# Optimization experiments

Measured on AMD Instinct MI355X. Metric: run time of the kernel, lower is better.

## Reference

```python
import math
import jax, jax.numpy as jnp
import numpy as np

B, L, D = 8, 4096, 512
FACTOR = 5


def setup_inputs() -> dict:
    key = jax.random.key(0)
    kq, kk, kv = jax.random.split(key, 3)
    q = jax.random.normal(kq, (B, L, D), dtype=jnp.float32)
    k = jax.random.normal(kk, (B, L, D), dtype=jnp.float32)
    v = jax.random.normal(kv, (B, L, D), dtype=jnp.float32)
    return {"q": q, "k": k, "v": v}


def reference(q, k, v):
    # ProbSparse attention (sparse=True branch, L_Q > 1)
    L_Q = q.shape[1]
    scale = q.shape[-1] ** -0.5
    # scores: [B, L_Q, L_K]
    scores = jnp.einsum('bqd,bkd->bqk', q, k) * scale
    # sparsity measure M = max - mean over keys: [B, L_Q]
    M = scores.max(axis=-1) - scores.mean(axis=-1)
    u = max(1, int(FACTOR * math.log(L_Q + 1)))
    u = min(u, L_Q)  # static python int (u = 41 here)
    _, top_idx = jax.lax.top_k(M, u)  # [B, u]
    # gather top-u query rows of scores, softmax over keys (row-wise softmax
    # commutes with row selection, so this matches softmax-then-gather)
    scores_top = jnp.take_along_axis(scores, top_idx[:, :, None], axis=1)  # [B, u, L_K]
    attn = jax.nn.softmax(scores_top, axis=-1)
    out_top = jnp.einsum('buk,bkd->bud', attn, v)  # [B, u, D]
    # non-selected queries receive the mean value
    v_mean = jnp.broadcast_to(v.mean(axis=1, keepdims=True), v.shape)  # [B, L, D]
    b_idx = jnp.arange(q.shape[0])[:, None]  # [B, 1]
    out = v_mean.at[b_idx, top_idx].set(out_top)
    return out
```

## Files before the change

### kernel.cpp

```cpp
#include <hip/hip_runtime.h>
#include <math.h>

#define B_ 8
#define L_ 4096
#define D_ 512
#define U_ 41
#define NSL 16

static constexpr float SCALE = 0.044194173824159216f;

typedef __attribute__((ext_vector_type(8))) short bf16x8;
typedef __attribute__((ext_vector_type(4))) float f32x4;
typedef unsigned int uint;


__global__ __launch_bounds__(512) void kSums1(const float* __restrict__ k,
                                              const float* __restrict__ v,
                                              float* __restrict__ partk,
                                              float* __restrict__ partv) {
  const int s = blockIdx.x;
  const int b = blockIdx.y;
  const int d = threadIdx.x;
  const int rows = L_ / NSL;
  const size_t base = ((size_t)b * L_ + (size_t)s * rows) * D_ + d;
  float ks = 0.f, vs = 0.f;
  for (int l = 0; l < rows; ++l) {
    ks += k[base + (size_t)l * D_];
    vs += v[base + (size_t)l * D_];
  }
  partk[(b * NSL + s) * D_ + d] = ks;
  partv[(b * NSL + s) * D_ + d] = vs;
}

__global__ __launch_bounds__(512) void kSums2(const float* __restrict__ partk,
                                              const float* __restrict__ partv,
                                              float* __restrict__ ksum,
                                              float* __restrict__ vmean) {
  const int b = blockIdx.x;
  const int d = threadIdx.x;
  float ks = 0.f, vs = 0.f;
  for (int s = 0; s < NSL; ++s) {
    ks += partk[(b * NSL + s) * D_ + d];
    vs += partv[(b * NSL + s) * D_ + d];
  }
  ksum[b * D_ + d] = ks;
  vmean[b * D_ + d] = vs * (1.f / L_);
}

__global__ __launch_bounds__(256) void kMeanM(const float* __restrict__ q,
                                              const float* __restrict__ ksum,
                                              const float* __restrict__ pmax,
                                              float* __restrict__ M) {
  __shared__ float ks[D_];
  const int gid = blockIdx.x * 256 + threadIdx.x;
  const int b = gid >> 12;
  for (int i = threadIdx.x; i < D_; i += 256) ks[i] = ksum[b * D_ + i];
  __syncthreads();
  const float* qp = q + (size_t)gid * D_;
  float acc = 0.f;
  for (int i = 0; i < D_; i += 4) {
    float4 t = *(const float4*)(qp + i);
    acc += t.x * ks[i] + t.y * ks[i + 1] + t.z * ks[i + 2] + t.w * ks[i + 3];
  }
  const float rowmax = fmaxf(pmax[gid], pmax[B_ * L_ + gid]);
  M[gid] = SCALE * (rowmax - acc * (1.f / L_));
}

__global__ __launch_bounds__(64) void kTopK2(const float* __restrict__ M,
                                             int* __restrict__ topidx) {
  __shared__ float vals[L_];
  const int b = blockIdx.x;
  const int lane = threadIdx.x;
  for (int i = lane; i < L_; i += 64) vals[i] = M[b * L_ + i];
  __syncthreads();
  for (int it = 0; it < U_; ++it) {
    float bv = -3.4e38f;
    int bi = 0x7fffffff;
    for (int i = lane; i < L_; i += 64) {
      float x = vals[i];
      if (x > bv) { bv = x; bi = i; }
    }
#pragma unroll
    for (int off = 1; off < 64; off <<= 1) {
      float ov = __shfl_xor(bv, off);
      int oi = __shfl_xor(bi, off);
      if (ov > bv || (ov == bv && oi < bi)) { bv = ov; bi = oi; }
    }
    if (lane == 0) { topidx[b * U_ + it] = bi; vals[bi] = -3.4e38f; }
    __syncthreads();
  }
}

__global__ __launch_bounds__(256) void kFill(const float* __restrict__ vmean,
                                             float* __restrict__ out) {
  const int g = blockIdx.x * 256 + threadIdx.x;
  const int d4 = g & 127;
  const int bl = g >> 7;
  const int b = bl >> 12;
  ((float4*)out)[g] = ((const float4*)vmean)[b * 128 + d4];
}

__device__ inline uint bf16_rne_bits(float x) {
  uint u = __builtin_bit_cast(uint, x);
  return (u + 0x7FFFu + ((u >> 16) & 1u)) >> 16;
}
__device__ inline float bits_to_f32(uint hi16) {
  return __builtin_bit_cast(float, hi16 << 16);
}

__global__ __launch_bounds__(256) void kConvert(const float* __restrict__ src,
                                                unsigned char* __restrict__ dhi,
                                                unsigned char* __restrict__ dlo) {
  const int cid = blockIdx.x * 256 + threadIdx.x;
  const int c16 = cid & 7;
  const int row = (cid >> 3) & 127;
  const int dsi = (cid >> 10) & 7;
  const int rt = (cid >> 13) & 31;
  const int b = cid >> 18;
  const int l = rt * 128 + row;
  const int d = dsi * 64 + c16 * 8;
  const float* sp = src + ((size_t)(b * L_ + l) * D_ + d);
  float x[8];
  *(float4*)(x) = *(const float4*)sp;
  *(float4*)(x + 4) = *(const float4*)(sp + 4);
  uint hw[4], lw[4];
#pragma unroll
  for (int p = 0; p < 4; ++p) {
    float a = x[2 * p], c = x[2 * p + 1];
    uint ha = bf16_rne_bits(a), hc = bf16_rne_bits(c);
    float ra = a - bits_to_f32(ha);
    float rc = c - bits_to_f32(hc);
    uint la = bf16_rne_bits(ra), lc = bf16_rne_bits(rc);
    hw[p] = ha | (hc << 16);
    lw[p] = la | (lc << 16);
  }
  const size_t dstByte = ((size_t)(cid >> 3) << 7) +
                         (uint)((c16 << 4) ^ ((row & 7) << 4));
  *(uint4*)(dhi + dstByte) = make_uint4(hw[0], hw[1], hw[2], hw[3]);
  *(uint4*)(dlo + dstByte) = make_uint4(lw[0], lw[1], lw[2], lw[3]);
}

__device__ __forceinline__ void gload16(const unsigned char* g, unsigned char* l) {
  __builtin_amdgcn_global_load_lds(
      (const __attribute__((address_space(1))) unsigned int*)(g),
      (__attribute__((address_space(3))) unsigned int*)(l), 16, 0, 0);
}

__global__ __launch_bounds__(256, 2) void kRowMaxB(const unsigned char* __restrict__ qhi,
                                                   const unsigned char* __restrict__ qlo,
                                                   const unsigned char* __restrict__ khi,
                                                   const unsigned char* __restrict__ klo,
                                                   float* __restrict__ pmax) {
  __shared__ unsigned char lds[65536];
  __shared__ float red[256];
  unsigned char* ldsQhi = lds;
  unsigned char* ldsQlo = lds + 16384;
  unsigned char* ldsKhi = lds + 32768;
  unsigned char* ldsKlo = lds + 49152;

  const int b = blockIdx.y;
  const int qt = blockIdx.x;
  const int kh = blockIdx.z;
  const int tid = threadIdx.x;
  const int lane = tid & 63;
  const int wave = tid >> 6;
  const int wq = wave >> 1, wk = wave & 1;

  const size_t qtb = ((size_t)((b * 32 + qt) * 8)) * 16384;
  const unsigned char* qhB = qhi + qtb;
  const unsigned char* qlB = qlo + qtb;

  float rmax[4][4];
#pragma unroll
  for (int i = 0; i < 4; ++i)
#pragma unroll
    for (int j = 0; j < 4; ++j) rmax[i][j] = -3.4e38f;

  for (int kt = 0; kt < 16; ++kt) {
    const size_t ktb = ((size_t)((b * 32 + (kh * 16 + kt)) * 8)) * 16384;
    const unsigned char* khB = khi + ktb;
    const unsigned char* klB = klo + ktb;

    f32x4 acc[4][4];
#pragma unroll
    for (int i = 0; i < 4; ++i)
#pragma unroll
      for (int j = 0; j < 4; ++j)
#pragma unroll
        for (int e = 0; e < 4; ++e) acc[i][j][e] = 0.f;

    for (int dsi = 0; dsi < 8; ++dsi) {
      __syncthreads();
      {
        const size_t dof = (size_t)dsi * 16384 + (size_t)tid * 16;
        const size_t lof = (size_t)tid * 16;
#pragma unroll
        for (int i = 0; i < 4; ++i) {
          gload16(qhB + dof + i * 4096, ldsQhi + lof + i * 4096);
          gload16(qlB + dof + i * 4096, ldsQlo + lof + i * 4096);
          gload16(khB + dof + i * 4096, ldsKhi + lof + i * 4096);
          gload16(klB + dof + i * 4096, ldsKlo + lof + i * 4096);
        }
      }
      __syncthreads();

#pragma unroll
      for (int h = 0; h < 2; ++h) {
        const int rbyte = h * 64 + ((lane >> 4) << 4);
        bf16x8 aH[4], aL[4], bH[4], bL[4];
#pragma unroll
        for (int f = 0; f < 4; ++f) {
          const int qrow = wq * 64 + f * 16 + (lane & 15);
          const int krow = wk * 64 + f * 16 + (lane & 15);
          const int qoff = qrow * 128 + (rbyte ^ ((qrow & 7) << 4));
          const int koff = krow * 128 + (rbyte ^ ((krow & 7) << 4));
          aH[f] = *(const bf16x8*)(ldsQhi + qoff);
          aL[f] = *(const bf16x8*)(ldsQlo + qoff);
          bH[f] = *(const bf16x8*)(ldsKhi + koff);
          bL[f] = *(const bf16x8*)(ldsKlo + koff);
        }
#pragma unroll
        for (int mf = 0; mf < 4; ++mf)
#pragma unroll
          for (int nf = 0; nf < 4; ++nf) {
            acc[mf][nf] = __builtin_amdgcn_mfma_f32_16x16x32_bf16(aH[mf], bH[nf], acc[mf][nf], 0, 0, 0);
            acc[mf][nf] = __builtin_amdgcn_mfma_f32_16x16x32_bf16(aH[mf], bL[nf], acc[mf][nf], 0, 0, 0);
            acc[mf][nf] = __builtin_amdgcn_mfma_f32_16x16x32_bf16(aL[mf], bH[nf], acc[mf][nf], 0, 0, 0);
          }
      }
    }
#pragma unroll
    for (int mf = 0; mf < 4; ++mf)
#pragma unroll
      for (int r = 0; r < 4; ++r) {
        float m = fmaxf(fmaxf(acc[mf][0][r], acc[mf][1][r]),
                        fmaxf(acc[mf][2][r], acc[mf][3][r]));
        rmax[mf][r] = fmaxf(rmax[mf][r], m);
      }
  }

#pragma unroll
  for (int mf = 0; mf < 4; ++mf)
#pragma unroll
    for (int r = 0; r < 4; ++r) {
      float v = rmax[mf][r];
#pragma unroll
      for (int off = 1; off < 16; off <<= 1) v = fmaxf(v, __shfl_xor(v, off));
      rmax[mf][r] = v;
    }

  if ((lane & 15) == 0) {
#pragma unroll
    for (int mf = 0; mf < 4; ++mf)
#pragma unroll
      for (int r = 0; r < 4; ++r) {
        const int rowl = wq * 64 + mf * 16 + ((lane >> 4) << 2) + r;
        red[wk * 128 + rowl] = rmax[mf][r];
      }
  }
  __syncthreads();
  if (tid < 128) {
    pmax[(size_t)kh * B_ * L_ + (size_t)b * L_ + blockIdx.x * 128 + tid] =
        fmaxf(red[tid], red[128 + tid]);
  }
}


__global__ __launch_bounds__(64) void kGatherQ(const float* __restrict__ q,
                                               const int* __restrict__ topidx,
                                               unsigned char* __restrict__ qselhi,
                                               unsigned char* __restrict__ qsello) {
  const int j = blockIdx.x;
  const int b = blockIdx.y;
  const int lane = threadIdx.x;
  const int dsi = lane >> 3;
  const int c16 = lane & 7;
  float x[8] = {0.f, 0.f, 0.f, 0.f, 0.f, 0.f, 0.f, 0.f};
  if (j < U_) {
    const int row = topidx[b * U_ + j];
    const float* sp = q + ((size_t)(b * L_ + row)) * D_ + dsi * 64 + c16 * 8;
    *(float4*)(x) = *(const float4*)sp;
    *(float4*)(x + 4) = *(const float4*)(sp + 4);
  }
  uint hw[4], lw[4];
#pragma unroll
  for (int p = 0; p < 4; ++p) {
    float a = x[2 * p], c = x[2 * p + 1];
    uint ha = bf16_rne_bits(a), hc = bf16_rne_bits(c);
    float ra = a - bits_to_f32(ha);
    float rc = c - bits_to_f32(hc);
    uint la = bf16_rne_bits(ra), lc = bf16_rne_bits(rc);
    hw[p] = ha | (hc << 16);
    lw[p] = la | (lc << 16);
  }
  const size_t dstByte = ((size_t)((b * 8 + dsi) * 64 + j)) * 128 +
                         (uint)((c16 << 4) ^ ((j & 7) << 4));
  *(uint4*)(qselhi + dstByte) = make_uint4(hw[0], hw[1], hw[2], hw[3]);
  *(uint4*)(qsello + dstByte) = make_uint4(lw[0], lw[1], lw[2], lw[3]);
}

__global__ __launch_bounds__(256) void kSelScoresM(const unsigned char* __restrict__ qselhi,
                                                   const unsigned char* __restrict__ qsello,
                                                   const unsigned char* __restrict__ khi,
                                                   const unsigned char* __restrict__ klo,
                                                   float* __restrict__ P) {
  __shared__ unsigned char lds[49152];
  unsigned char* ldsQhi = lds;
  unsigned char* ldsQlo = lds + 8192;
  unsigned char* ldsKhi = lds + 16384;
  unsigned char* ldsKlo = lds + 32768;

  const int kc = blockIdx.x;
  const int b = blockIdx.y;
  const int tid = threadIdx.x;
  const int lane = tid & 63;
  const int wave = tid >> 6;
  const int wq = wave >> 1, wk = wave & 1;

  const size_t ktb = ((size_t)((b * 32 + kc) * 8)) * 16384;
  const unsigned char* khB = khi + ktb;
  const unsigned char* klB = klo + ktb;
  const size_t qb = ((size_t)b * 8) * 8192;
  const unsigned char* qhB = qselhi + qb;
  const unsigned char* qlB = qsello + qb;

  f32x4 acc[2][4];
#pragma unroll
  for (int i = 0; i < 2; ++i)
#pragma unroll
    for (int j = 0; j < 4; ++j)
#pragma unroll
      for (int e = 0; e < 4; ++e) acc[i][j][e] = 0.f;

  for (int dsi = 0; dsi < 8; ++dsi) {
    __syncthreads();
    {
      const size_t qof = (size_t)dsi * 8192 + (size_t)tid * 16;
      const size_t kof = (size_t)dsi * 16384 + (size_t)tid * 16;
      const size_t lof = (size_t)tid * 16;
#pragma unroll
      for (int i = 0; i < 2; ++i) {
        gload16(qhB + qof + i * 4096, ldsQhi + lof + i * 4096);
        gload16(qlB + qof + i * 4096, ldsQlo + lof + i * 4096);
      }
#pragma unroll
      for (int i = 0; i < 4; ++i) {
        gload16(khB + kof + i * 4096, ldsKhi + lof + i * 4096);
        gload16(klB + kof + i * 4096, ldsKlo + lof + i * 4096);
      }
    }
    __syncthreads();

#pragma unroll
    for (int h = 0; h < 2; ++h) {
      const int rbyte = h * 64 + ((lane >> 4) << 4);
      bf16x8 aH[2], aL[2], bH[4], bL[4];
#pragma unroll
      for (int f = 0; f < 2; ++f) {
        const int qrow = wq * 32 + f * 16 + (lane & 15);
        const int qoff = qrow * 128 + (rbyte ^ ((qrow & 7) << 4));
        aH[f] = *(const bf16x8*)(ldsQhi + qoff);
        aL[f] = *(const bf16x8*)(ldsQlo + qoff);
      }
#pragma unroll
      for (int f = 0; f < 4; ++f) {
        const int krow = wk * 64 + f * 16 + (lane & 15);
        const int koff = krow * 128 + (rbyte ^ ((krow & 7) << 4));
        bH[f] = *(const bf16x8*)(ldsKhi + koff);
        bL[f] = *(const bf16x8*)(ldsKlo + koff);
      }
#pragma unroll
      for (int mf = 0; mf < 2; ++mf)
#pragma unroll
        for (int nf = 0; nf < 4; ++nf) {
          acc[mf][nf] = __builtin_amdgcn_mfma_f32_16x16x32_bf16(aH[mf], bH[nf], acc[mf][nf], 0, 0, 0);
          acc[mf][nf] = __builtin_amdgcn_mfma_f32_16x16x32_bf16(aH[mf], bL[nf], acc[mf][nf], 0, 0, 0);
          acc[mf][nf] = __builtin_amdgcn_mfma_f32_16x16x32_bf16(aL[mf], bH[nf], acc[mf][nf], 0, 0, 0);
        }
    }
  }

#pragma unroll
  for (int mf = 0; mf < 2; ++mf)
#pragma unroll
    for (int nf = 0; nf < 4; ++nf)
#pragma unroll
      for (int r = 0; r < 4; ++r) {
        const int row = wq * 32 + mf * 16 + ((lane >> 4) << 2) + r;
        const int key = kc * 128 + wk * 64 + nf * 16 + (lane & 15);
        if (row < U_)
          P[((size_t)(b * U_ + row)) * L_ + key] = acc[mf][nf][r];
      }
}

__global__ __launch_bounds__(256) void kSoftmaxP(float* __restrict__ P) {
  __shared__ float red[256];
  const int j = blockIdx.x, b = blockIdx.y;
  float* row = P + ((size_t)(b * U_ + j)) * L_;
  const int tid = threadIdx.x;
  float v[16];
  float mx = -3.4e38f;
#pragma unroll
  for (int i = 0; i < 16; ++i) {
    v[i] = row[tid + i * 256];
    mx = fmaxf(mx, v[i]);
  }
  red[tid] = mx;
  __syncthreads();
  for (int s = 128; s > 0; s >>= 1) {
    if (tid < s) red[tid] = fmaxf(red[tid], red[tid + s]);
    __syncthreads();
  }
  mx = red[0];
  __syncthreads();
  float sum = 0.f;
#pragma unroll
  for (int i = 0; i < 16; ++i) {
    float e = expf((v[i] - mx) * SCALE);
    v[i] = e;
    sum += e;
  }
  red[tid] = sum;
  __syncthreads();
  for (int s = 128; s > 0; s >>= 1) {
    if (tid < s) red[tid] += red[tid + s];
    __syncthreads();
  }
  const float inv = 1.f / red[0];
#pragma unroll
  for (int i = 0; i < 16; ++i) row[tid + i * 256] = v[i] * inv;
}

__global__ __launch_bounds__(256) void kPV(const float* __restrict__ P,
                                           const float* __restrict__ v,
                                           float* __restrict__ partial) {
  __shared__ float plds[41 * 128];
  const int kc = blockIdx.x;
  const int dc = blockIdx.y;
  const int b = blockIdx.z;
  const int tid = threadIdx.x;
  const int trow = tid >> 7, dcol = tid & 127;
  float acc[U_];
#pragma unroll
  for (int j = 0; j < U_; ++j) acc[j] = 0.f;

  for (int sub = 0; sub < 4; ++sub) {
    const int key0 = kc * 512 + sub * 128;
    __syncthreads();
    for (int idx = tid; idx < U_ * 128; idx += 256)
      plds[idx] = P[((size_t)(b * U_ + (idx >> 7))) * L_ + key0 + (idx & 127)];
    __syncthreads();
    const float* vp = v + ((size_t)(b * L_ + key0 + trow * 64)) * D_ + dc * 128 + dcol;
    float vv[64];
#pragma unroll
    for (int kk = 0; kk < 64; ++kk) vv[kk] = vp[(size_t)kk * D_];
#pragma unroll
    for (int j = 0; j < U_; ++j) {
      const float4* pr = (const float4*)&plds[j * 128 + trow * 64];
      float a = acc[j];
#pragma unroll
      for (int q4 = 0; q4 < 16; ++q4) {
        float4 p4 = pr[q4];
        a = fmaf(p4.x, vv[q4 * 4 + 0], a);
        a = fmaf(p4.y, vv[q4 * 4 + 1], a);
        a = fmaf(p4.z, vv[q4 * 4 + 2], a);
        a = fmaf(p4.w, vv[q4 * 4 + 3], a);
      }
      acc[j] = a;
    }
  }
  float* pp = partial + ((size_t)((b * 4 + dc) * 16 + kc * 2 + trow)) * (U_ * 128) + dcol;
#pragma unroll
  for (int j = 0; j < U_; ++j) pp[j * 128] = acc[j];
}

__global__ __launch_bounds__(256) void kPVout(const float* __restrict__ partial,
                                              const int* __restrict__ topidx,
                                              float* __restrict__ out) {
  const int j = blockIdx.x, b = blockIdx.y;
  const int tid = threadIdx.x;
  const int l = topidx[b * U_ + j];
#pragma unroll
  for (int h = 0; h < 2; ++h) {
    const int d = tid + h * 256;
    const int dc = d >> 7, dcol = d & 127;
    float s = 0.f;
#pragma unroll
    for (int part = 0; part < 16; ++part)
      s += partial[((size_t)((b * 4 + dc) * 16 + part)) * (U_ * 128) + j * 128 + dcol];
    out[((size_t)(b * L_ + l)) * D_ + d] = s;
  }
}


__device__ inline void stageHalfRow(const float* __restrict__ src,
                                    char* hiBase, char* loBase,
                                    int row, int shalf) {
  const int sw = (row & 7) << 4;
  char* hp = hiBase + row * 128;
  char* lp = loBase + row * 128;
#pragma unroll
  for (int g = 0; g < 4; ++g) {
    f32x4 x0 = *(const f32x4*)(src + g * 8);
    f32x4 x1 = *(const f32x4*)(src + g * 8 + 4);
    float x[8] = {x0.x, x0.y, x0.z, x0.w, x1.x, x1.y, x1.z, x1.w};
    uint hw[4], lw[4];
#pragma unroll
    for (int p = 0; p < 4; ++p) {
      float a = x[2 * p], c = x[2 * p + 1];
      uint ha = bf16_rne_bits(a), hc = bf16_rne_bits(c);
      float ra = a - bits_to_f32(ha);
      float rc = c - bits_to_f32(hc);
      uint la = bf16_rne_bits(ra), lc = bf16_rne_bits(rc);
      hw[p] = ha | (hc << 16);
      lw[p] = la | (lc << 16);
    }
    const int off = (shalf * 64 + g * 16) ^ sw;
    *(uint4*)(hp + off) = make_uint4(hw[0], hw[1], hw[2], hw[3]);
    *(uint4*)(lp + off) = make_uint4(lw[0], lw[1], lw[2], lw[3]);
  }
}

__global__ __launch_bounds__(256, 2) void kRowMaxM(const float* __restrict__ q,
                                                   const float* __restrict__ k,
                                                   float* __restrict__ pmax) {
  __shared__ char lds[65536];
  __shared__ float red[256];
  char* ldsQhi = lds;
  char* ldsQlo = lds + 16384;
  char* ldsKhi = lds + 32768;
  char* ldsKlo = lds + 49152;

  const int b = blockIdx.y;
  const int qbase = blockIdx.x * 128;
  const int kh = blockIdx.z;
  const int tid = threadIdx.x;
  const int lane = tid & 63;
  const int wave = tid >> 6;
  const int wq = wave >> 1, wk = wave & 1;
  const int srow = tid >> 1;
  const int shalf = tid & 1;

  const float* qrow_base = q + ((size_t)b * L_ + qbase + srow) * D_ + shalf * 32;
  const float* krow_base = k + ((size_t)b * L_ + kh * 2048 + srow) * D_ + shalf * 32;

  float rmax[4][4];
#pragma unroll
  for (int i = 0; i < 4; ++i)
#pragma unroll
    for (int j = 0; j < 4; ++j) rmax[i][j] = -3.4e38f;

  for (int kt = 0; kt < 16; ++kt) {
    f32x4 acc[4][4];
#pragma unroll
    for (int i = 0; i < 4; ++i)
#pragma unroll
      for (int j = 0; j < 4; ++j)
#pragma unroll
        for (int e = 0; e < 4; ++e) acc[i][j][e] = 0.f;

    for (int dsi = 0; dsi < 8; ++dsi) {
      __syncthreads();
      stageHalfRow(qrow_base + dsi * 64, ldsQhi, ldsQlo, srow, shalf);
      stageHalfRow(krow_base + (size_t)kt * 128 * D_ + dsi * 64, ldsKhi, ldsKlo, srow, shalf);
      __syncthreads();

#pragma unroll
      for (int h = 0; h < 2; ++h) {
        const int rbyte = h * 64 + ((lane >> 4) << 4);
        bf16x8 aH[4], aL[4], bH[4], bL[4];
#pragma unroll
        for (int f = 0; f < 4; ++f) {
          const int qrow = wq * 64 + f * 16 + (lane & 15);
          const int krow = wk * 64 + f * 16 + (lane & 15);
          const int qoff = qrow * 128 + (rbyte ^ ((qrow & 7) << 4));
          const int koff = krow * 128 + (rbyte ^ ((krow & 7) << 4));
          aH[f] = *(const bf16x8*)(ldsQhi + qoff);
          aL[f] = *(const bf16x8*)(ldsQlo + qoff);
          bH[f] = *(const bf16x8*)(ldsKhi + koff);
          bL[f] = *(const bf16x8*)(ldsKlo + koff);
        }
#pragma unroll
        for (int mf = 0; mf < 4; ++mf)
#pragma unroll
          for (int nf = 0; nf < 4; ++nf) {
            acc[mf][nf] = __builtin_amdgcn_mfma_f32_16x16x32_bf16(aH[mf], bH[nf], acc[mf][nf], 0, 0, 0);
            acc[mf][nf] = __builtin_amdgcn_mfma_f32_16x16x32_bf16(aH[mf], bL[nf], acc[mf][nf], 0, 0, 0);
            acc[mf][nf] = __builtin_amdgcn_mfma_f32_16x16x32_bf16(aL[mf], bH[nf], acc[mf][nf], 0, 0, 0);
          }
      }
    }
#pragma unroll
    for (int mf = 0; mf < 4; ++mf)
#pragma unroll
      for (int r = 0; r < 4; ++r) {
        float m = fmaxf(fmaxf(acc[mf][0][r], acc[mf][1][r]),
                        fmaxf(acc[mf][2][r], acc[mf][3][r]));
        rmax[mf][r] = fmaxf(rmax[mf][r], m);
      }
  }

#pragma unroll
  for (int mf = 0; mf < 4; ++mf)
#pragma unroll
    for (int r = 0; r < 4; ++r) {
      float v = rmax[mf][r];
#pragma unroll
      for (int off = 1; off < 16; off <<= 1) v = fmaxf(v, __shfl_xor(v, off));
      rmax[mf][r] = v;
    }

  if ((lane & 15) == 0) {
#pragma unroll
    for (int mf = 0; mf < 4; ++mf)
#pragma unroll
      for (int r = 0; r < 4; ++r) {
        const int rowl = wq * 64 + mf * 16 + ((lane >> 4) << 2) + r;
        red[wk * 128 + rowl] = rmax[mf][r];
      }
  }
  __syncthreads();
  if (tid < 128) {
    pmax[(size_t)kh * B_ * L_ + (size_t)b * L_ + qbase + tid] =
        fmaxf(red[tid], red[128 + tid]);
  }
}

__global__ __launch_bounds__(256) void kAttnSel(const float* __restrict__ q,
                                                const float* __restrict__ k,
                                                const float* __restrict__ v,
                                                const int* __restrict__ topidx,
                                                float* __restrict__ out) {
  __shared__ float qs[D_];
  __shared__ float sc[L_];
  __shared__ float wred[4];
  __shared__ float sred[256];
  const int b = blockIdx.y;
  const int l_sel = topidx[b * U_ + blockIdx.x];
  const int tid = threadIdx.x;
  const int wave = tid >> 6, lane = tid & 63;
  const float* qrow = q + ((size_t)b * L_ + l_sel) * D_;
  qs[tid] = qrow[tid];
  qs[tid + 256] = qrow[tid + 256];
  __syncthreads();
  float qr[8];
#pragma unroll
  for (int i = 0; i < 8; ++i) qr[i] = qs[lane * 8 + i];
  float wmax = -3.4e38f;
  for (int l = wave; l < L_; l += 4) {
    const float* kp = k + ((size_t)b * L_ + l) * D_ + lane * 8;
    float4 k0 = *(const float4*)kp;
    float4 k1 = *(const float4*)(kp + 4);
    float p = k0.x * qr[0] + k0.y * qr[1] + k0.z * qr[2] + k0.w * qr[3] +
              k1.x * qr[4] + k1.y * qr[5] + k1.z * qr[6] + k1.w * qr[7];
#pragma unroll
    for (int off = 32; off > 0; off >>= 1) p += __shfl_xor(p, off);
    if (lane == 0) sc[l] = p;
    wmax = fmaxf(wmax, p);
  }
  if (lane == 0) wred[wave] = wmax;
  __syncthreads();
  const float mx = fmaxf(fmaxf(wred[0], wred[1]), fmaxf(wred[2], wred[3]));
  float psum = 0.f;
  for (int i = tid; i < L_; i += 256) {
    float e = expf((sc[i] - mx) * SCALE);
    sc[i] = e;
    psum += e;
  }
  sred[tid] = psum;
  __syncthreads();
  for (int s = 128; s > 0; s >>= 1) {
    if (tid < s) sred[tid] += sred[tid + s];
    __syncthreads();
  }
  const float inv = 1.f / sred[0];
  float a0a = 0.f, a0b = 0.f, a1a = 0.f, a1b = 0.f;
  const float* vb = v + (size_t)b * L_ * D_;
  for (int l = 0; l < L_; l += 2) {
    float p0 = sc[l], p1 = sc[l + 1];
    const float* vp0 = vb + (size_t)l * D_;
    const float* vp1 = vp0 + D_;
    a0a = fmaf(p0, vp0[tid], a0a);
    a1a = fmaf(p0, vp0[tid + 256], a1a);
    a0b = fmaf(p1, vp1[tid], a0b);
    a1b = fmaf(p1, vp1[tid + 256], a1b);
  }
  float* orow = out + ((size_t)b * L_ + l_sel) * D_;
  orow[tid] = (a0a + a0b) * inv;
  orow[tid + 256] = (a1a + a1b) * inv;
}


extern "C" void kernel_launch(void* const* d_in, const int* in_sizes, int n_in,
                              void* d_out, int out_size, void* d_ws, size_t ws_size,
                              hipStream_t stream) {
  const float* q = (const float*)d_in[0];
  const float* k = (const float*)d_in[1];
  const float* v = (const float*)d_in[2];
  float* out = (float*)d_out;
  unsigned char* wsb = (unsigned char*)d_ws;

  const size_t NEED = 84183040;

  if (ws_size >= NEED) {
    unsigned char* qhiW = wsb;
    unsigned char* qloW = wsb + 33554432;
    float* pmax = (float*)(wsb + 67108864);
    float* Marr = (float*)(wsb + 67371008);
    float* ksum = (float*)(wsb + 67502080);
    float* vmean = (float*)(wsb + 67518464);
    int* tidx = (int*)(wsb + 67534848);
    float* partk = (float*)(wsb + 67536896);
    float* partv = (float*)(wsb + 67799040);
    float* P = (float*)(wsb + 68061184);
    float* partial = (float*)(wsb + 73435136);
    unsigned char* qselhi = (unsigned char*)partial;
    unsigned char* qsello = qselhi + 524288;
    unsigned char* khiO = (unsigned char*)d_out;
    unsigned char* kloO = khiO + 33554432;

    kConvert<<<8192, 256, 0, stream>>>(q, qhiW, qloW);
    kConvert<<<8192, 256, 0, stream>>>(k, khiO, kloO);
    kSums1<<<dim3(NSL, B_), 512, 0, stream>>>(k, v, partk, partv);
    kSums2<<<B_, 512, 0, stream>>>(partk, partv, ksum, vmean);
    kRowMaxB<<<dim3(L_ / 128, B_, 2), 256, 0, stream>>>(qhiW, qloW, khiO, kloO, pmax);
    kMeanM<<<B_ * L_ / 256, 256, 0, stream>>>(q, ksum, pmax, Marr);
    kTopK2<<<B_, 64, 0, stream>>>(Marr, tidx);
    kGatherQ<<<dim3(64, B_), 64, 0, stream>>>(q, tidx, qselhi, qsello);
    kSelScoresM<<<dim3(32, B_), 256, 0, stream>>>(qselhi, qsello, khiO, kloO, P);
    kSoftmaxP<<<dim3(U_, B_), 256, 0, stream>>>(P);
    kFill<<<B_ * L_ * D_ / 1024, 256, 0, stream>>>(vmean, out);
    kPV<<<dim3(8, 4, B_), 256, 0, stream>>>(P, v, partial);
    kPVout<<<dim3(U_, B_), 256, 0, stream>>>(partial, tidx, out);
  } else {
    float* ws = (float*)d_ws;
    float* Marr = ws;
    float* pmax = ws + 32768;
    float* ksum = ws + 98304;
    float* vmean = ws + 102400;
    int* tidx = (int*)(ws + 106496);
    float* partk = ws + 107008;
    float* partv = ws + 107008 + B_ * NSL * D_;

    kSums1<<<dim3(NSL, B_), 512, 0, stream>>>(k, v, partk, partv);
    kSums2<<<B_, 512, 0, stream>>>(partk, partv, ksum, vmean);
    kRowMaxM<<<dim3(L_ / 128, B_, 2), 256, 0, stream>>>(q, k, pmax);
    kMeanM<<<B_ * L_ / 256, 256, 0, stream>>>(q, ksum, pmax, Marr);
    kTopK2<<<B_, 64, 0, stream>>>(Marr, tidx);
    kFill<<<B_ * L_ * D_ / 1024, 256, 0, stream>>>(vmean, out);
    kAttnSel<<<dim3(U_, B_), 256, 0, stream>>>(q, k, v, tidx, out);
  }
}
```

Baseline: 685.9 us.

## Double-buffer row-max GEMM loads, swizzle workgroups, and register-resident top-k

```diff
diff --git a/kernel.cpp b/kernel.cpp
--- a/kernel.cpp
+++ b/kernel.cpp
@@ -66,28 +66,56 @@
   M[gid] = SCALE * (rowmax - acc * (1.f / L_));
 }
 
-__global__ __launch_bounds__(64) void kTopK2(const float* __restrict__ M,
-                                             int* __restrict__ topidx) {
-  __shared__ float vals[L_];
+__global__ __launch_bounds__(256) void kTopK3(const float* __restrict__ M,
+                                              int* __restrict__ topidx) {
+  __shared__ float wv[2][4];
+  __shared__ int wi[2][4];
   const int b = blockIdx.x;
-  const int lane = threadIdx.x;
-  for (int i = lane; i < L_; i += 64) vals[i] = M[b * L_ + i];
-  __syncthreads();
+  const int tid = threadIdx.x;
+  const int wave = tid >> 6, lane = tid & 63;
+  float v[16];
+#pragma unroll
+  for (int j = 0; j < 16; ++j) v[j] = M[b * L_ + tid + j * 256];
+  float bv = v[0];
+  int bj = 0;
+#pragma unroll
+  for (int j = 1; j < 16; ++j)
+    if (v[j] > bv) { bv = v[j]; bj = j; }
+  int bi = tid + bj * 256;
+
   for (int it = 0; it < U_; ++it) {
-    float bv = -3.4e38f;
-    int bi = 0x7fffffff;
-    for (int i = lane; i < L_; i += 64) {
-      float x = vals[i];
-      if (x > bv) { bv = x; bi = i; }
-    }
+    float rv = bv;
+    int ri = bi;
 #pragma unroll
     for (int off = 1; off < 64; off <<= 1) {
-      float ov = __shfl_xor(bv, off);
-      int oi = __shfl_xor(bi, off);
-      if (ov > bv || (ov == bv && oi < bi)) { bv = ov; bi = oi; }
-    }
-    if (lane == 0) { topidx[b * U_ + it] = bi; vals[bi] = -3.4e38f; }
-    __syncthreads();
+      float ov = __shfl_xor(rv, off);
+      int oi = __shfl_xor(ri, off);
+      if (ov > rv || (ov == rv && oi < ri)) { rv = ov; ri = oi; }
+    }
+    const int par = it & 1;
+    if (lane == 0) { wv[par][wave] = rv; wi[par][wave] = ri; }
+    __syncthreads();
+    float gv = wv[par][0];
+    int gi = wi[par][0];
+#pragma unroll
+    for (int w = 1; w < 4; ++w) {
+      float ov = wv[par][w];
+      int oi = wi[par][w];
+      if (ov > gv || (ov == gv && oi < gi)) { gv = ov; gi = oi; }
+    }
+    if (tid == 0) topidx[b * U_ + it] = gi;
+    if (gi == bi) {
+      const int jb = gi >> 8;
+#pragma unroll
+      for (int j = 0; j < 16; ++j)
+        if (j == jb) v[j] = -3.4e38f;
+      bv = v[0];
+      bj = 0;
+#pragma unroll
+      for (int j = 1; j < 16; ++j)
+        if (v[j] > bv) { bv = v[j]; bj = j; }
+      bi = tid + bj * 256;
+    }
   }
 }
 
@@ -146,97 +174,101 @@
       (__attribute__((address_space(3))) unsigned int*)(l), 16, 0, 0);
 }
 
-__global__ __launch_bounds__(256, 2) void kRowMaxB(const unsigned char* __restrict__ qhi,
+__global__ __launch_bounds__(256, 1) void kRowMaxC(const unsigned char* __restrict__ qhi,
                                                    const unsigned char* __restrict__ qlo,
                                                    const unsigned char* __restrict__ khi,
                                                    const unsigned char* __restrict__ klo,
                                                    float* __restrict__ pmax) {
-  __shared__ unsigned char lds[65536];
-  __shared__ float red[256];
-  unsigned char* ldsQhi = lds;
-  unsigned char* ldsQlo = lds + 16384;
-  unsigned char* ldsKhi = lds + 32768;
-  unsigned char* ldsKlo = lds + 49152;
-
-  const int b = blockIdx.y;
-  const int qt = blockIdx.x;
-  const int kh = blockIdx.z;
+  __shared__ unsigned char lds[131072];
+
+  const int wg = blockIdx.x;
+  const int swz = (wg & 7) * 64 + (wg >> 3);
+  const int qt = swz & 31;
+  const int b = (swz >> 5) & 7;
+  const int kh = swz >> 8;
+
   const int tid = threadIdx.x;
   const int lane = tid & 63;
   const int wave = tid >> 6;
   const int wq = wave >> 1, wk = wave & 1;
 
-  const size_t qtb = ((size_t)((b * 32 + qt) * 8)) * 16384;
-  const unsigned char* qhB = qhi + qtb;
-  const unsigned char* qlB = qlo + qtb;
+  const unsigned char* qhB = qhi + ((size_t)((b * 32 + qt) * 8)) * 16384;
+  const unsigned char* qlB = qlo + ((size_t)((b * 32 + qt) * 8)) * 16384;
+  const size_t kbase = ((size_t)((b * 32 + kh * 16) * 8)) * 16384;
+  const unsigned char* khB = khi + kbase;
+  const unsigned char* klB = klo + kbase;
+
+  const size_t lof = (size_t)tid * 16;
+
+  auto STAGE = [&](int s, unsigned char* buf) {
+    const int dsi = s & 7;
+    const size_t qof = (size_t)dsi * 16384 + lof;
+    const size_t kof = (size_t)s * 16384 + lof;
+#pragma unroll
+    for (int i = 0; i < 4; ++i) {
+      gload16(qhB + qof + i * 4096, buf + lof + i * 4096);
+      gload16(qlB + qof + i * 4096, buf + 16384 + lof + i * 4096);
+      gload16(khB + kof + i * 4096, buf + 32768 + lof + i * 4096);
+      gload16(klB + kof + i * 4096, buf + 49152 + lof + i * 4096);
+    }
+  };
 
   float rmax[4][4];
+  f32x4 acc[4][4];
 #pragma unroll
   for (int i = 0; i < 4; ++i)
 #pragma unroll
-    for (int j = 0; j < 4; ++j) rmax[i][j] = -3.4e38f;
-
-  for (int kt = 0; kt < 16; ++kt) {
-    const size_t ktb = ((size_t)((b * 32 + (kh * 16 + kt)) * 8)) * 16384;
-    const unsigned char* khB = khi + ktb;
-    const unsigned char* klB = klo + ktb;
-
-    f32x4 acc[4][4];
-#pragma unroll
-    for (int i = 0; i < 4; ++i)
-#pragma unroll
-      for (int j = 0; j < 4; ++j)
-#pragma unroll
-        for (int e = 0; e < 4; ++e) acc[i][j][e] = 0.f;
-
-    for (int dsi = 0; dsi < 8; ++dsi) {
-      __syncthreads();
-      {
-        const size_t dof = (size_t)dsi * 16384 + (size_t)tid * 16;
-        const size_t lof = (size_t)tid * 16;
-#pragma unroll
-        for (int i = 0; i < 4; ++i) {
-          gload16(qhB + dof + i * 4096, ldsQhi + lof + i * 4096);
-          gload16(qlB + dof + i * 4096, ldsQlo + lof + i * 4096);
-          gload16(khB + dof + i * 4096, ldsKhi + lof + i * 4096);
-          gload16(klB + dof + i * 4096, ldsKlo + lof + i * 4096);
+    for (int j = 0; j < 4; ++j) {
+      rmax[i][j] = -3.4e38f;
+#pragma unroll
+      for (int e = 0; e < 4; ++e) acc[i][j][e] = 0.f;
+    }
+
+  auto PHASE = [&](int s, const unsigned char* bufR, unsigned char* bufW) {
+    __syncthreads();
+    if (s < 127) STAGE(s + 1, bufW);
+#pragma unroll
+    for (int h = 0; h < 2; ++h) {
+      const int rbyte = h * 64 + ((lane >> 4) << 4);
+      bf16x8 aH[4], aL[4], bH[4], bL[4];
+#pragma unroll
+      for (int f = 0; f < 4; ++f) {
+        const int qrow = wq * 64 + f * 16 + (lane & 15);
+        const int krow = wk * 64 + f * 16 + (lane & 15);
+        const int qoff = qrow * 128 + (rbyte ^ ((qrow & 7) << 4));
+        const int koff = krow * 128 + (rbyte ^ ((krow & 7) << 4));
+        aH[f] = *(const bf16x8*)(bufR + qoff);
+        aL[f] = *(const bf16x8*)(bufR + 16384 + qoff);
+        bH[f] = *(const bf16x8*)(bufR + 32768 + koff);
+        bL[f] = *(const bf16x8*)(bufR + 49152 + koff);
+      }
+#pragma unroll
+      for (int mf = 0; mf < 4; ++mf)
+#pragma unroll
+        for (int nf = 0; nf < 4; ++nf) {
+          acc[mf][nf] = __builtin_amdgcn_mfma_f32_16x16x32_bf16(aH[mf], bH[nf], acc[mf][nf], 0, 0, 0);
+          acc[mf][nf] = __builtin_amdgcn_mfma_f32_16x16x32_bf16(aH[mf], bL[nf], acc[mf][nf], 0, 0, 0);
+          acc[mf][nf] = __builtin_amdgcn_mfma_f32_16x16x32_bf16(aL[mf], bH[nf], acc[mf][nf], 0, 0, 0);
         }
-      }
-      __syncthreads();
-
-#pragma unroll
-      for (int h = 0; h < 2; ++h) {
-        const int rbyte = h * 64 + ((lane >> 4) << 4);
-        bf16x8 aH[4], aL[4], bH[4], bL[4];
-#pragma unroll
-        for (int f = 0; f < 4; ++f) {
-          const int qrow = wq * 64 + f * 16 + (lane & 15);
-          const int krow = wk * 64 + f * 16 + (lane & 15);
-          const int qoff = qrow * 128 + (rbyte ^ ((qrow & 7) << 4));
-          const int koff = krow * 128 + (rbyte ^ ((krow & 7) << 4));
-          aH[f] = *(const bf16x8*)(ldsQhi + qoff);
-          aL[f] = *(const bf16x8*)(ldsQlo + qoff);
-          bH[f] = *(const bf16x8*)(ldsKhi + koff);
-          bL[f] = *(const bf16x8*)(ldsKlo + koff);
+    }
+    if ((s & 7) == 7) {
+#pragma unroll
+      for (int mf = 0; mf < 4; ++mf)
+#pragma unroll
+        for (int r = 0; r < 4; ++r) {
+          float m = fmaxf(fmaxf(acc[mf][0][r], acc[mf][1][r]),
+                          fmaxf(acc[mf][2][r], acc[mf][3][r]));
+          rmax[mf][r] = fmaxf(rmax[mf][r], m);
+#pragma unroll
+          for (int nf = 0; nf < 4; ++nf) acc[mf][nf][r] = 0.f;
         }
-#pragma unroll
-        for (int mf = 0; mf < 4; ++mf)
-#pragma unroll
-          for (int nf = 0; nf < 4; ++nf) {
-            acc[mf][nf] = __builtin_amdgcn_mfma_f32_16x16x32_bf16(aH[mf], bH[nf], acc[mf][nf], 0, 0, 0);
-            acc[mf][nf] = __builtin_amdgcn_mfma_f32_16x16x32_bf16(aH[mf], bL[nf], acc[mf][nf], 0, 0, 0);
-            acc[mf][nf] = __builtin_amdgcn_mfma_f32_16x16x32_bf16(aL[mf], bH[nf], acc[mf][nf], 0, 0, 0);
-          }
-      }
-    }
-#pragma unroll
-    for (int mf = 0; mf < 4; ++mf)
-#pragma unroll
-      for (int r = 0; r < 4; ++r) {
-        float m = fmaxf(fmaxf(acc[mf][0][r], acc[mf][1][r]),
-                        fmaxf(acc[mf][2][r], acc[mf][3][r]));
-        rmax[mf][r] = fmaxf(rmax[mf][r], m);
-      }
+    }
+  };
+
+  STAGE(0, lds);
+  for (int s = 0; s < 128; s += 2) {
+    PHASE(s, lds, lds + 65536);
+    PHASE(s + 1, lds + 65536, lds);
   }
 
 #pragma unroll
@@ -249,6 +281,8 @@
       rmax[mf][r] = v;
     }
 
+  __syncthreads();
+  float* red = (float*)lds;
   if ((lane & 15) == 0) {
 #pragma unroll
     for (int mf = 0; mf < 4; ++mf)
@@ -260,7 +294,7 @@
   }
   __syncthreads();
   if (tid < 128) {
-    pmax[(size_t)kh * B_ * L_ + (size_t)b * L_ + blockIdx.x * 128 + tid] =
+    pmax[(size_t)kh * B_ * L_ + (size_t)b * L_ + qt * 128 + tid] =
         fmaxf(red[tid], red[128 + tid]);
   }
 }
@@ -723,9 +757,9 @@
     kConvert<<<8192, 256, 0, stream>>>(k, khiO, kloO);
     kSums1<<<dim3(NSL, B_), 512, 0, stream>>>(k, v, partk, partv);
     kSums2<<<B_, 512, 0, stream>>>(partk, partv, ksum, vmean);
-    kRowMaxB<<<dim3(L_ / 128, B_, 2), 256, 0, stream>>>(qhiW, qloW, khiO, kloO, pmax);
+    kRowMaxC<<<512, 256, 0, stream>>>(qhiW, qloW, khiO, kloO, pmax);
     kMeanM<<<B_ * L_ / 256, 256, 0, stream>>>(q, ksum, pmax, Marr);
-    kTopK2<<<B_, 64, 0, stream>>>(Marr, tidx);
+    kTopK3<<<B_, 256, 0, stream>>>(Marr, tidx);
     kGatherQ<<<dim3(64, B_), 64, 0, stream>>>(q, tidx, qselhi, qsello);
     kSelScoresM<<<dim3(32, B_), 256, 0, stream>>>(qselhi, qsello, khiO, kloO, P);
     kSoftmaxP<<<dim3(U_, B_), 256, 0, stream>>>(P);
@@ -746,7 +780,7 @@
     kSums2<<<B_, 512, 0, stream>>>(partk, partv, ksum, vmean);
     kRowMaxM<<<dim3(L_ / 128, B_, 2), 256, 0, stream>>>(q, k, pmax);
     kMeanM<<<B_ * L_ / 256, 256, 0, stream>>>(q, ksum, pmax, Marr);
-    kTopK2<<<B_, 64, 0, stream>>>(Marr, tidx);
+    kTopK3<<<B_, 256, 0, stream>>>(Marr, tidx);
     kFill<<<B_ * L_ * D_ / 1024, 256, 0, stream>>>(vmean, out);
     kAttnSel<<<dim3(U_, B_), 256, 0, stream>>>(q, k, v, tidx, out);
   }
```

After: 677.7 us. Within noise of the previous version (-1.2%).
